# Kernel optimization log

Measured on AMD Instinct MI355X. Metric: run time of the kernel, lower is better.

Reference implementation:

```python
import jax, jax.numpy as jnp
import numpy as np

N_E, E_DIM = 8192, 256
COMMIT = 0.25
DECAY = 0.95
EPS = 1e-05


def setup_inputs() -> dict:
    key = jax.random.key(0)
    k1, k2, k3 = jax.random.split(key, 3)
    x = jax.random.normal(k1, (8, 256, 16, 16, 16), dtype=jnp.float32)
    codebook = jax.random.normal(k2, (N_E, E_DIM), dtype=jnp.float32)
    ema_count = jnp.zeros((N_E,), dtype=jnp.float32)
    ema_weight = jax.random.normal(k3, (N_E, E_DIM), dtype=jnp.float32)
    return {"x": x, "codebook": codebook, "ema_count": ema_count, "ema_weight": ema_weight}


def reference(x, codebook, ema_count, ema_weight):
    b, c, h, w, l = x.shape
    K = codebook.shape[0]
    # 'b c h w l -> (b h w l) c'
    flat_x = jnp.transpose(x, (0, 2, 3, 4, 1)).reshape(-1, c)  # [N, c]
    N = flat_x.shape[0]

    # squared L2 distances via the expanded form (matmul-dominated)
    distances = (jnp.sum(flat_x ** 2, axis=1, keepdims=True)
                 + jnp.sum(codebook ** 2, axis=1)
                 - 2.0 * flat_x @ codebook.T)  # [N, K]
    idx = jnp.argmin(distances, axis=1)  # [N]

    # quantized = one_hot(idx) @ codebook == gather
    quant_flat = codebook[idx]  # [N, c]

    # EMA update (training branch); one-hot column sums == segment sums
    counts = jax.ops.segment_sum(jnp.ones((N,), dtype=x.dtype), idx, num_segments=K)
    new_count = ema_count * DECAY + (1.0 - DECAY) * counts
    new_count = (new_count + EPS) / (b + K * EPS) * b
    dw = jax.ops.segment_sum(flat_x, idx, num_segments=K)  # encodings.T @ flat_x
    new_weight = ema_weight * DECAY + (1.0 - DECAY) * dw
    new_codebook = new_weight / new_count[:, None]

    e_loss = COMMIT * jnp.mean((jax.lax.stop_gradient(quant_flat) - flat_x) ** 2)

    # straight-through estimator
    quant_st = flat_x + jax.lax.stop_gradient(quant_flat - flat_x)
    quantized = jnp.transpose(quant_st.reshape(b, h, w, l, c), (0, 4, 1, 2, 3))

    avg_probs = counts / N
    perplexity = jnp.exp(-jnp.sum(avg_probs * jnp.log(avg_probs + 1e-10)))
    unique = jnp.count_nonzero(counts)

    return (quantized, e_loss, perplexity, unique,
            new_codebook, new_count, new_weight, idx)
```

## Files before the change

### kernel.cpp

```cpp
#include <hip/hip_runtime.h>
#include <hip/hip_bf16.h>
#include <stdint.h>

#define N_ROWS 32768
#define K_CODES 8192
#define C_DIM 256
#define DECAYF 0.95f
#define COMMITF 0.25f
#define EPSF 1e-5f
#define RESC_KEYGAP 2u
#define RESC_CAP 16384

#define OFF_QUANT 0
#define OFF_ELOSS 8388608
#define OFF_PERP  8388609
#define OFF_UNIQ  8388610
#define OFF_NCB   8388611
#define OFF_NCNT  10485763
#define OFF_NW    10493955
#define OFF_IDX   12591107

typedef float f32x4 __attribute__((ext_vector_type(4)));
typedef int i32x4 __attribute__((ext_vector_type(4)));
typedef unsigned long long u64;
typedef unsigned int u32;

#define SWZ(r) ((((r) >> 2) & 7) << 2)

#if defined(__has_builtin)
#if __has_builtin(__builtin_amdgcn_global_load_lds)
#define HAVE_GLDS 1
#endif
#endif
#ifdef HAVE_GLDS
#define GLDS16(g, l) __builtin_amdgcn_global_load_lds( \
    (const __attribute__((address_space(1))) void*)(uintptr_t)(g), \
    (__attribute__((address_space(3))) void*)(uint32_t)(uintptr_t)(l), 16, 0, 0)
#else
#define GLDS16(g, l) do { *(float4*)(l) = *(const float4*)(g); } while (0)
#endif

__device__ __forceinline__ uint32_t fkey(float f) {
    uint32_t b = __float_as_uint(f);
    return b ^ ((uint32_t)((int32_t)b >> 31) | 0x80000000u);
}
__device__ __forceinline__ void enc8(float v, float inv, signed char& h, signed char& l) {
    int q = __float2int_rn(v * inv);
    q = q > 16319 ? 16319 : (q < -16320 ? -16320 : q);
    int hh = (q + 64) >> 7;
    h = (signed char)hh;
    l = (signed char)(q - (hh << 7));
}

__global__ __launch_bounds__(256)
void kmax(const float* __restrict__ x, const float* __restrict__ cb, float* __restrict__ maxbuf) {
    const int bid = blockIdx.x, t = threadIdx.x;
    const float* src = bid < 2048 ? x : cb;
    const size_t base = bid < 2048 ? (size_t)bid * 4096 : (size_t)(bid - 2048) * 4096;
    float m = 0.f;
    #pragma unroll
    for (int i = 0; i < 4; ++i) {
        const float4 v = *(const float4*)(src + base + ((size_t)i * 256 + t) * 4);
        m = fmaxf(m, fmaxf(fmaxf(fabsf(v.x), fabsf(v.y)), fmaxf(fabsf(v.z), fabsf(v.w))));
    }
    #pragma unroll
    for (int off = 32; off; off >>= 1) m = fmaxf(m, __shfl_down(m, off));
    __shared__ float ps[4];
    if ((t & 63) == 0) ps[t >> 6] = m;
    __syncthreads();
    if (t == 0) maxbuf[bid] = fmaxf(fmaxf(ps[0], ps[1]), fmaxf(ps[2], ps[3]));
}

__global__ void kscale(const float* __restrict__ maxbuf, float* __restrict__ scl,
                       float* __restrict__ counts, float* __restrict__ loss_arr,
                       unsigned* __restrict__ rcnt) {
    const int t = threadIdx.x;
    float mx = 0.f, me = 0.f;
    for (int i = t; i < 2048; i += 256) mx = fmaxf(mx, maxbuf[i]);
    for (int i = 2048 + t; i < 2560; i += 256) me = fmaxf(me, maxbuf[i]);
    #pragma unroll
    for (int off = 32; off; off >>= 1) {
        mx = fmaxf(mx, __shfl_down(mx, off));
        me = fmaxf(me, __shfl_down(me, off));
    }
    __shared__ float px[4], pe[4];
    if ((t & 63) == 0) { px[t >> 6] = mx; pe[t >> 6] = me; }
    __syncthreads();
    if (t == 0) {
        const float Sx = fmaxf(fmaxf(px[0], px[1]), fmaxf(px[2], px[3])) * (16384.f / 16320.f) + 1e-20f;
        const float Se = fmaxf(fmaxf(pe[0], pe[1]), fmaxf(pe[2], pe[3])) * (16384.f / 16320.f) + 1e-20f;
        scl[0] = Sx; scl[1] = Se; scl[2] = Sx * Se / 268435456.f;
        *rcnt = 0u;
    }
    for (int i = t; i < K_CODES; i += 256) counts[i] = 0.f;
    loss_arr[t] = 0.f;
}

__global__ __launch_bounds__(256)
void kprep(const float* __restrict__ cb, const float* __restrict__ x,
           signed char* __restrict__ Ah, signed char* __restrict__ Al,
           signed char* __restrict__ Bh, signed char* __restrict__ Bl,
           float* __restrict__ cnorm, const float* __restrict__ scl) {
    const int bid = blockIdx.x;
    const int t = threadIdx.x;
    if (bid < 2048) {
        const float inve = 16384.f / scl[1];
        const size_t i4 = ((size_t)bid * 256 + t) * 4;
        const float4 v = *(const float4*)(cb + i4);
        signed char h0, h1, h2, h3, l0, l1, l2, l3;
        enc8(v.x, inve, h0, l0); enc8(v.y, inve, h1, l1);
        enc8(v.z, inve, h2, l2); enc8(v.w, inve, h3, l3);
        *(char4*)(Bh + i4) = make_char4(h0, h1, h2, h3);
        *(char4*)(Bl + i4) = make_char4(l0, l1, l2, l3);
        float s = v.x * v.x + v.y * v.y + v.z * v.z + v.w * v.w;
        #pragma unroll
        for (int off = 32; off; off >>= 1) s += __shfl_down(s, off);
        if ((t & 63) == 0) cnorm[i4 >> 8] = s;
    } else {
        const float invx = 16384.f / scl[0];
        __shared__ float xt[64][65];
        const int xb_id = bid - 2048;
        const int st = xb_id & 63;
        const int ct = (xb_id >> 6) & 3;
        const int b  = xb_id >> 8;
        const float* xb = x + ((size_t)b * C_DIM + ct * 64) * 4096 + st * 64;
        {
            const int s_l = t & 63, c0 = t >> 6;
            #pragma unroll
            for (int cc = 0; cc < 16; ++cc) {
                int c_l = cc * 4 + c0;
                xt[c_l][s_l] = xb[(size_t)c_l * 4096 + s_l];
            }
        }
        __syncthreads();
        const int c2 = (t & 31) * 2;
        const int s0 = t >> 5;
        #pragma unroll
        for (int ww = 0; ww < 8; ++ww) {
            int s_o = ww * 8 + s0;
            signed char h0, l0, h1, l1;
            enc8(xt[c2][s_o], invx, h0, l0);
            enc8(xt[c2 + 1][s_o], invx, h1, l1);
            size_t off = ((size_t)(b * 4096 + st * 64 + s_o)) * C_DIM + ct * 64 + c2;
            *(char2*)(Ah + off) = make_char2(h0, h1);
            *(char2*)(Al + off) = make_char2(l0, l1);
        }
    }
}

__global__ __launch_bounds__(512, 4)
void kargmin_i8(const signed char* __restrict__ Ah, const signed char* __restrict__ Al,
                const signed char* __restrict__ Bh, const signed char* __restrict__ Bl,
                const float* __restrict__ cnorm, const float* __restrict__ scl,
                uint2* __restrict__ wsmin) {
    __shared__ unsigned char As[3][128 * 64];
    __shared__ unsigned char Bs[3][256 * 64];

    const int t = threadIdx.x;
    const int lane = t & 63;
    const int wid = t >> 6;
    const int xcd = blockIdx.x & 7;
    const int ii = blockIdx.x >> 3;
    const int ntile = xcd * 4 + (ii & 3);
    const int mtile = ii >> 2;
    const int m0 = mtile * 128;
    const int n0 = ntile * 256;
    const int wr = wid >> 2;
    const int wc = wid & 3;
    const int wm = wr * 64;
    const int wn = wc * 64;
    const int lm = lane & 15;
    const int lh = lane >> 4;

    i32x4 acc[4][4];
    #pragma unroll
    for (int i = 0; i < 4; ++i)
        #pragma unroll
        for (int j = 0; j < 4; ++j) acc[i][j] = (i32x4){0, 0, 0, 0};

    const int sAr = t >> 2;
    const int ssl = t & 3;
    const int gsA = ssl ^ (sAr & 3) ^ ((sAr >> 2) & 3);
    const size_t thr = (size_t)sAr * 256 + (size_t)gsA * 16;

    const signed char* pA0 = Ah + (size_t)m0 * 256 + thr;
    const signed char* pA1 = Al + (size_t)m0 * 256 + thr;
    const signed char* pB0 = Bh + (size_t)n0 * 256 + thr;
    const signed char* pB1 = Bl + (size_t)n0 * 256 + thr;

#define STAGE(PA, PB, KOFF, BUF) do { \
        GLDS16((PA) + (KOFF), &As[BUF][t * 16]); \
        GLDS16((PB) + (KOFF), &Bs[BUF][t * 16]); \
        GLDS16((PB) + 32768 + (KOFF), &Bs[BUF][(512 + t) * 16]); \
    } while (0)

#define BARN(N) do { \
        asm volatile("s_waitcnt vmcnt(" #N ")" ::: "memory"); \
        __builtin_amdgcn_sched_barrier(0); \
        __builtin_amdgcn_s_barrier(); \
        __builtin_amdgcn_sched_barrier(0); \
    } while (0)

    const int rboff = (lh ^ (lm & 3) ^ ((lm >> 2) & 3)) * 16;

#define TILEC(CUR, PF, FOLD) do { \
        PF; \
        i32x4 a_[4], b_[4]; \
        _Pragma("unroll") \
        for (int j = 0; j < 4; ++j) \
            b_[j] = *(const i32x4*)&Bs[CUR][(wn + j * 16 + lm) * 64 + rboff]; \
        _Pragma("unroll") \
        for (int i = 0; i < 4; ++i) \
            a_[i] = *(const i32x4*)&As[CUR][(wm + i * 16 + lm) * 64 + rboff]; \
        _Pragma("unroll") \
        for (int i = 0; i < 4; ++i) \
            _Pragma("unroll") \
            for (int j = 0; j < 4; ++j) \
                acc[i][j] = __builtin_amdgcn_mfma_i32_16x16x64_i8(a_[i], b_[j], acc[i][j], 0, 0, 0); \
        FOLD; \
    } while (0)

#define FOLDACC \
        _Pragma("unroll") \
        for (int i = 0; i < 4; ++i) \
            _Pragma("unroll") \
            for (int j = 0; j < 4; ++j) \
                acc[i][j] = acc[i][j] << 7

    STAGE(pA0, pB0, 0, 0);
    STAGE(pA0, pB0, 64, 1);
    BARN(3);
    TILEC(0, STAGE(pA0, pB0, 128, 2), (void)0);  BARN(3);
    TILEC(1, STAGE(pA0, pB0, 192, 0), (void)0);  BARN(3);
    TILEC(2, STAGE(pA0, pB1,   0, 1), (void)0);  BARN(3);
    TILEC(0, STAGE(pA0, pB1,  64, 2), FOLDACC);  BARN(3);
    TILEC(1, STAGE(pA0, pB1, 128, 0), (void)0);  BARN(3);
    TILEC(2, STAGE(pA0, pB1, 192, 1), (void)0);  BARN(3);
    TILEC(0, STAGE(pA1, pB0,   0, 2), (void)0);  BARN(3);
    TILEC(1, STAGE(pA1, pB0,  64, 0), (void)0);  BARN(3);
    TILEC(2, STAGE(pA1, pB0, 128, 1), (void)0);  BARN(3);
    TILEC(0, STAGE(pA1, pB0, 192, 2), (void)0);  BARN(3);
    TILEC(1, (void)0, (void)0);                  BARN(0);
    TILEC(2, (void)0, (void)0);
#undef TILEC
#undef STAGE
#undef BARN
#undef FOLDACC
    __syncthreads();

    const float invu = 1.f / (256.f * scl[2]);
    int cni[4];
    #pragma unroll
    for (int j = 0; j < 4; ++j)
        cni[j] = (int)rintf(cnorm[n0 + wn + j * 16 + lm] * invu) + 0x20000000;

    u32* redbuf = (u32*)&As[0][0];
    #pragma unroll
    for (int i = 0; i < 4; ++i) {
        u32 p1[4], p2[4];
        #pragma unroll
        for (int r = 0; r < 4; ++r) {
            u32 b1 = ~0u, b2 = ~0u;
            #pragma unroll
            for (int j = 0; j < 4; ++j) {
                const u32 v = (u32)(cni[j] - acc[i][j][r]);
                const u32 key = ((v >> 10) << 8) | (u32)(wn + j * 16 + lm);
                if (key < b1) { b2 = b1; b1 = key; }
                else if (key < b2) b2 = key;
            }
            p1[r] = b1; p2[r] = b2;
        }
        #pragma unroll
        for (int off = 1; off < 16; off <<= 1) {
            #pragma unroll
            for (int r = 0; r < 4; ++r) {
                const u32 o1 = __shfl_xor(p1[r], off);
                const u32 o2 = __shfl_xor(p2[r], off);
                const u32 lo = min(p1[r], o1);
                const u32 hi = max(p1[r], o1);
                p1[r] = lo;
                p2[r] = min(hi, min(p2[r], o2));
            }
        }
        if (lm == 0) {
            #pragma unroll
            for (int r = 0; r < 4; ++r) {
                const int rl = wm + i * 16 + lh * 4 + r;
                redbuf[rl * 8 + wc * 2 + 0] = p1[r];
                redbuf[rl * 8 + wc * 2 + 1] = p2[r];
            }
        }
    }
    __syncthreads();
    if (t < 128) {
        u32 m1 = ~0u, m2 = ~0u;
        #pragma unroll
        for (int w = 0; w < 4; ++w) {
            const u32 a1 = redbuf[t * 8 + w * 2 + 0];
            const u32 a2 = redbuf[t * 8 + w * 2 + 1];
            const u32 lo = min(m1, a1);
            const u32 hi = max(m1, a1);
            m1 = lo;
            m2 = min(hi, min(m2, a2));
        }
        wsmin[(size_t)(m0 + t) * 32 + ntile] = make_uint2(m1, m2);
    }
}

__global__ void kcombine(const uint2* __restrict__ wsmin, float* __restrict__ idxf,
                         unsigned* __restrict__ rcnt, unsigned* __restrict__ rrows,
                         uint2* __restrict__ rpair, float* __restrict__ counts) {
    const int row = blockIdx.x * 256 + threadIdx.x;
    const uint2* p = wsmin + (size_t)row * 32;
    u32 m1 = ~0u, m2 = ~0u;
    int nt1 = 0, nt2 = 0;
    for (int nt = 0; nt < 32; ++nt) {
        const uint2 c = p[nt];
        if (c.x < m1) { m2 = m1; nt2 = nt1; m1 = c.x; nt1 = nt; }
        else if (c.x < m2) { m2 = c.x; nt2 = nt; }
        if (c.y < m2) { m2 = c.y; nt2 = nt; }
    }
    const int k = nt1 * 256 + (int)(m1 & 255u);
    idxf[row] = (float)k;
    atomicAdd(&counts[k], 1.0f);
    if ((m2 >> 8) - (m1 >> 8) <= RESC_KEYGAP) {
        unsigned slot = atomicAdd(rcnt, 1u);
        if (slot < RESC_CAP) {
            rrows[slot] = (unsigned)row;
            rpair[slot] = make_uint2((unsigned)k, (unsigned)(nt2 * 256 + (int)(m2 & 255u)));
        }
    }
}

__global__ __launch_bounds__(256)
void krescue2(const float* __restrict__ x, const float* __restrict__ cb,
              const float* __restrict__ cnorm, const unsigned* __restrict__ rcnt,
              const unsigned* __restrict__ rrows, const uint2* __restrict__ rpair,
              float* __restrict__ idxf, float* __restrict__ counts) {
    const int lane = threadIdx.x & 63;
    const int wv = threadIdx.x >> 6;
    unsigned cnt = *rcnt; if (cnt > RESC_CAP) cnt = RESC_CAP;
    for (unsigned i = blockIdx.x * 4 + wv; i < cnt; i += gridDim.x * 4) {
        const int row = (int)rrows[i];
        const uint2 kk = rpair[i];
        const int b = row >> 12, s = row & 4095;
        float d1 = 0.f, d2 = 0.f;
        #pragma unroll
        for (int q = 0; q < 4; ++q) {
            const int c = lane + q * 64;
            const float xv = x[((size_t)(b * 256 + c)) * 4096 + s];
            d1 = fmaf(xv, cb[(size_t)kk.x * 256 + c], d1);
            d2 = fmaf(xv, cb[(size_t)kk.y * 256 + c], d2);
        }
        #pragma unroll
        for (int off = 32; off; off >>= 1) {
            d1 += __shfl_down(d1, off);
            d2 += __shfl_down(d2, off);
        }
        if (lane == 0) {
            const float dist1 = fmaf(-2.f, d1, cnorm[kk.x]);
            const float dist2 = fmaf(-2.f, d2, cnorm[kk.y]);
            const u64 p1 = ((u64)fkey(dist1) << 32) | kk.x;
            const u64 p2 = ((u64)fkey(dist2) << 32) | kk.y;
            const int knew = (int)(unsigned)((p1 < p2 ? p1 : p2) & 0xffffffffu);
            const int kold = (int)kk.x;
            if (knew != kold) {
                atomicAdd(&counts[kold], -1.0f);
                atomicAdd(&counts[knew], 1.0f);
                idxf[row] = (float)knew;
            }
        }
    }
}

__global__ void kscan(const float* __restrict__ counts, unsigned* __restrict__ off,
                      unsigned* __restrict__ cursor) {
    __shared__ unsigned part[256];
    const int t = threadIdx.x;
    unsigned local[32];
    unsigned s = 0;
    #pragma unroll
    for (int i = 0; i < 32; ++i) { local[i] = s; s += (unsigned)counts[t * 32 + i]; }
    part[t] = s;
    __syncthreads();
    if (t == 0) {
        unsigned run = 0;
        for (int i = 0; i < 256; ++i) { unsigned v = part[i]; part[i] = run; run += v; }
    }
    __syncthreads();
    const unsigned base = part[t];
    #pragma unroll
    for (int i = 0; i < 32; ++i) {
        unsigned o = base + local[i];
        off[t * 32 + i] = o;
        cursor[t * 32 + i] = o;
    }
}

__global__ void kscatter(const float* __restrict__ idxf, unsigned* __restrict__ cursor,
                         unsigned* __restrict__ rowlist) {
    const int n = blockIdx.x * 256 + threadIdx.x;
    const int k = (int)idxf[n];
    unsigned pos = atomicAdd(&cursor[k], 1u);
    rowlist[pos] = (unsigned)n;
}

__global__ __launch_bounds__(256)
void kquant2(const float* __restrict__ x, const float* __restrict__ cb,
             const float* __restrict__ idxf, float* __restrict__ qout,
             float* __restrict__ loss_arr) {
    __shared__ int ki[64];
    __shared__ float cbt[64][257];
    const int t = threadIdx.x;
    const int bid = blockIdx.x;
    const int chunk = bid & 63;
    const int b = bid >> 6;
    const int s0 = chunk * 64;
    if (t < 64) ki[t] = (int)idxf[b * 4096 + s0 + t];
    __syncthreads();
    {
        const int lane = t & 63;
        const int rr = t >> 6;
        #pragma unroll
        for (int p = 0; p < 16; ++p) {
            const int r = p * 4 + rr;
            const float4 v = *(const float4*)(cb + (size_t)ki[r] * C_DIM + lane * 4);
            cbt[r][lane * 4 + 0] = v.x;
            cbt[r][lane * 4 + 1] = v.y;
            cbt[r][lane * 4 + 2] = v.z;
            cbt[r][lane * 4 + 3] = v.w;
        }
    }
    __syncthreads();
    const int sg = t & 15;
    const int c0 = t >> 4;
    float lsum = 0.f;
    #pragma unroll
    for (int cc = 0; cc < 16; ++cc) {
        const int c = cc * 16 + c0;
        const size_t go = ((size_t)b * C_DIM + c) * 4096 + s0 + sg * 4;
        const float4 xv = *(const float4*)(x + go);
        float qx = cbt[sg * 4 + 0][c];
        float qy = cbt[sg * 4 + 1][c];
        float qz = cbt[sg * 4 + 2][c];
        float qw = cbt[sg * 4 + 3][c];
        float4 st;
        st.x = xv.x + (qx - xv.x);
        st.y = xv.y + (qy - xv.y);
        st.z = xv.z + (qz - xv.z);
        st.w = xv.w + (qw - xv.w);
        *(float4*)(qout + go) = st;
        float dx = qx - xv.x, dy = qy - xv.y, dz = qz - xv.z, dw_ = qw - xv.w;
        lsum += dx * dx + dy * dy + dz * dz + dw_ * dw_;
    }
    #pragma unroll
    for (int off = 32; off; off >>= 1) lsum += __shfl_down(lsum, off);
    __shared__ float ps[4];
    if ((t & 63) == 0) ps[t >> 6] = lsum;
    __syncthreads();
    if (t == 0) atomicAdd(&loss_arr[bid & 255], ps[0] + ps[1] + ps[2] + ps[3]);
}

__global__ void kfinal3(const float* __restrict__ ema_c, const float* __restrict__ ema_w,
                        const float* __restrict__ counts, const unsigned* __restrict__ off,
                        const unsigned* __restrict__ rowlist,
                        const signed char* __restrict__ Ah, const signed char* __restrict__ Al,
                        const float* __restrict__ scl,
                        float* __restrict__ nw, float* __restrict__ ncb,
                        float* __restrict__ ncnt_out,
                        const float* __restrict__ loss_arr, float* __restrict__ out) {
    const int k = blockIdx.x;
    const int t = threadIdx.x;
    if (k < K_CODES) {
        const int cnt = (int)counts[k];
        const unsigned base = off[k];
        int a = 0;
        for (int i = 0; i < cnt; ++i) {
            const unsigned row = rowlist[base + i];
            a += (int)Ah[(size_t)row * C_DIM + t] * 128 + (int)Al[(size_t)row * C_DIM + t];
        }
        const float dwv = (float)a * (scl[0] * (1.f / 16384.f));
        const float ncnt = (DECAYF * ema_c[k] + (1.f - DECAYF) * counts[k] + EPSF)
                           / (8.f + (float)K_CODES * EPSF) * 8.f;
        const size_t o = (size_t)k * C_DIM + t;
        const float nwv = DECAYF * ema_w[o] + (1.f - DECAYF) * dwv;
        nw[o]  = nwv;
        ncb[o] = nwv / ncnt;
        if (t == 0) ncnt_out[k] = ncnt;
    } else {
        float nz = 0.f, s = 0.f;
        for (int kk = t; kk < K_CODES; kk += 256) {
            float cnt = counts[kk];
            if (cnt != 0.f) nz += 1.f;
            float p = cnt * (1.f / 32768.f);
            s += p * logf(p + 1e-10f);
        }
        float ls = loss_arr[t];
        #pragma unroll
        for (int off_ = 32; off_; off_ >>= 1) {
            s  += __shfl_down(s, off_);
            nz += __shfl_down(nz, off_);
            ls += __shfl_down(ls, off_);
        }
        __shared__ float ss[4], zz[4], ll[4];
        const int wid = t >> 6, lane = t & 63;
        if (lane == 0) { ss[wid] = s; zz[wid] = nz; ll[wid] = ls; }
        __syncthreads();
        if (t == 0) {
            float st = ss[0] + ss[1] + ss[2] + ss[3];
            float zt = zz[0] + zz[1] + zz[2] + zz[3];
            float lt = ll[0] + ll[1] + ll[2] + ll[3];
            out[OFF_ELOSS] = COMMITF * lt / 8388608.f;
            out[OFF_PERP]  = expf(-st);
            out[OFF_UNIQ]  = zt;
        }
    }
}

__global__ void knorm(const float* __restrict__ cb, float* __restrict__ cnorm) {
    const int wid  = threadIdx.x >> 6;
    const int lane = threadIdx.x & 63;
    const int row  = blockIdx.x * 4 + wid;
    const float4 v = *(const float4*)(cb + (size_t)row * C_DIM + lane * 4);
    float s = v.x * v.x + v.y * v.y + v.z * v.z + v.w * v.w;
    #pragma unroll
    for (int off = 32; off; off >>= 1) s += __shfl_down(s, off);
    if (lane == 0) cnorm[row] = s;
}

__launch_bounds__(256, 1)
__global__ void kargmin_fp32(const float* __restrict__ x, const float* __restrict__ cb,
                             const float* __restrict__ cnorm, float* __restrict__ idxf) {
    __shared__ float xs[64][256];
    __shared__ float es[64][256];
    const int t  = threadIdx.x;
    const int n0 = blockIdx.x * 64;
    const int b  = n0 >> 12;
    const int s0 = n0 & 4095;
    {
        const int r  = t & 63;
        const int c0 = t >> 6;
        const float* xb = x + (size_t)b * C_DIM * 4096 + s0 + r;
        const int sw = SWZ(r);
        #pragma unroll 8
        for (int cc = 0; cc < 64; ++cc) {
            int c = cc * 4 + c0;
            xs[r][c ^ sw] = xb[(size_t)c * 4096];
        }
    }
    const int mg  = t >> 4;
    const int ng  = t & 15;
    const int m0  = mg * 4;
    const int nn0 = ng * 4;
    const int swm = SWZ(m0);
    const int swn = SWZ(nn0);
    float minv[4] = {1e30f, 1e30f, 1e30f, 1e30f};
    int   mini[4] = {0, 0, 0, 0};
    for (int k0 = 0; k0 < K_CODES; k0 += 64) {
        __syncthreads();
        {
            const int lane = t & 63;
            const int cw   = t >> 6;
            #pragma unroll
            for (int p = 0; p < 16; ++p) {
                int code = p * 4 + cw;
                float4 v = *(const float4*)(cb + (size_t)(k0 + code) * C_DIM + lane * 4);
                *(float4*)&es[code][(lane * 4) ^ SWZ(code)] = v;
            }
        }
        float cn[4];
        #pragma unroll
        for (int j = 0; j < 4; ++j) cn[j] = cnorm[k0 + nn0 + j];
        __syncthreads();
        float acc[4][4];
        #pragma unroll
        for (int i = 0; i < 4; ++i)
            #pragma unroll
            for (int j = 0; j < 4; ++j) acc[i][j] = 0.f;
        #pragma unroll 4
        for (int c = 0; c < C_DIM; c += 4) {
            float4 xa[4], eb[4];
            #pragma unroll
            for (int i = 0; i < 4; ++i) xa[i] = *(const float4*)&xs[m0 + i][c ^ swm];
            #pragma unroll
            for (int j = 0; j < 4; ++j) eb[j] = *(const float4*)&es[nn0 + j][c ^ swn];
            #pragma unroll
            for (int i = 0; i < 4; ++i)
                #pragma unroll
                for (int j = 0; j < 4; ++j)
                    acc[i][j] += xa[i].x * eb[j].x + xa[i].y * eb[j].y +
                                 xa[i].z * eb[j].z + xa[i].w * eb[j].w;
        }
        #pragma unroll
        for (int j = 0; j < 4; ++j) {
            const int kg = k0 + nn0 + j;
            #pragma unroll
            for (int i = 0; i < 4; ++i) {
                float dist = fmaf(-2.f, acc[i][j], cn[j]);
                if (dist < minv[i]) { minv[i] = dist; mini[i] = kg; }
            }
        }
    }
    #pragma unroll
    for (int off = 1; off < 16; off <<= 1) {
        #pragma unroll
        for (int i = 0; i < 4; ++i) {
            float ov = __shfl_xor(minv[i], off);
            int   oi = __shfl_xor(mini[i], off);
            if (ov < minv[i] || (ov == minv[i] && oi < mini[i])) { minv[i] = ov; mini[i] = oi; }
        }
    }
    if (ng == 0) {
        #pragma unroll
        for (int i = 0; i < 4; ++i) idxf[n0 + m0 + i] = (float)mini[i];
    }
}

__global__ void kquant_legacy(const float* __restrict__ x, const float* __restrict__ cb,
                              const float* __restrict__ idxf, float* __restrict__ qout,
                              float* __restrict__ dw, float* __restrict__ counts,
                              float* __restrict__ loss_arr) {
    const int t   = threadIdx.x;
    const int bid = blockIdx.x;
    const int sc  = bid & 15;
    const int c   = (bid >> 4) & 255;
    const int b   = bid >> 12;
    const int s   = sc * 256 + t;
    const int n   = b * 4096 + s;
    const int k   = (int)idxf[n];
    const size_t xoff = ((size_t)b * C_DIM + c) * 4096 + s;
    const float xv = x[xoff];
    const float q  = cb[(size_t)k * C_DIM + c];
    qout[xoff] = xv + (q - xv);
    atomicAdd(&dw[(size_t)k * C_DIM + c], xv);
    if (c == 0) atomicAdd(&counts[k], 1.0f);
    float d = q - xv;
    float p = d * d;
    #pragma unroll
    for (int off = 32; off; off >>= 1) p += __shfl_down(p, off);
    __shared__ float ps[4];
    if ((t & 63) == 0) ps[t >> 6] = p;
    __syncthreads();
    if (t == 0) atomicAdd(&loss_arr[bid & 255], ps[0] + ps[1] + ps[2] + ps[3]);
}

__global__ void kstats_legacy(const float* __restrict__ counts, const float* __restrict__ loss_arr,
                              float* __restrict__ out) {
    const int t = threadIdx.x;
    float nz = 0.f, s = 0.f;
    for (int k = t; k < K_CODES; k += 256) {
        float cnt = counts[k];
        if (cnt != 0.f) nz += 1.f;
        float p = cnt * (1.f / 32768.f);
        s += p * logf(p + 1e-10f);
    }
    float ls = loss_arr[t];
    #pragma unroll
    for (int off = 32; off; off >>= 1) {
        s  += __shfl_down(s, off);
        nz += __shfl_down(nz, off);
        ls += __shfl_down(ls, off);
    }
    __shared__ float ss[4], zz[4], ll[4];
    const int wid = t >> 6, lane = t & 63;
    if (lane == 0) { ss[wid] = s; zz[wid] = nz; ll[wid] = ls; }
    __syncthreads();
    if (t == 0) {
        out[OFF_ELOSS] = COMMITF * (ll[0] + ll[1] + ll[2] + ll[3]) / 8388608.f;
        out[OFF_PERP]  = expf(-(ss[0] + ss[1] + ss[2] + ss[3]));
        out[OFF_UNIQ]  = zz[0] + zz[1] + zz[2] + zz[3];
    }
}

__global__ void kfinal_legacy(const float* __restrict__ ema_c, const float* __restrict__ ema_w,
                              float* __restrict__ counts, float* __restrict__ dw,
                              float* __restrict__ ncb) {
    const int k = blockIdx.x;
    const int c = threadIdx.x;
    const float cnt  = counts[k];
    const float ncnt = (DECAYF * ema_c[k] + (1.f - DECAYF) * cnt + EPSF)
                       / (8.f + (float)K_CODES * EPSF) * 8.f;
    const size_t o = (size_t)k * C_DIM + c;
    const float nw = DECAYF * ema_w[o] + (1.f - DECAYF) * dw[o];
    __syncthreads();
    dw[o]  = nw;
    ncb[o] = nw / ncnt;
    if (c == 0) counts[k] = ncnt;
}

extern "C" void kernel_launch(void* const* d_in, const int* in_sizes, int n_in,
                              void* d_out, int out_size, void* d_ws, size_t ws_size,
                              hipStream_t stream) {
    const float* x     = (const float*)d_in[0];
    const float* cb    = (const float*)d_in[1];
    const float* ema_c = (const float*)d_in[2];
    const float* ema_w = (const float*)d_in[3];
    float* out = (float*)d_out;

    float* qout = out + OFF_QUANT;
    float* ncb  = out + OFF_NCB;
    float* ncnt = out + OFF_NCNT;
    float* nw   = out + OFF_NW;
    float* idxf = out + OFF_IDX;

    const size_t szA = (size_t)N_ROWS * C_DIM;
    const size_t szB = (size_t)K_CODES * C_DIM;
    const size_t fcount = 8192 + 256 + 8192 + 4 + 2560;
    const size_t need = 2 * szA + 2 * szB + fcount * 4
                      + RESC_CAP * 8 + RESC_CAP * 4 + 4 + 8192 * 4 * 2 + 32768 * 4 + 64;
    const bool use_i8 = ws_size >= need;

    if (use_i8) {
        signed char* Ah = (signed char*)d_ws;
        signed char* Al = Ah + szA;
        signed char* Bh = Al + szA;
        signed char* Bl = Bh + szB;
        float* fbase      = (float*)(Bl + szB);
        float* cnorm      = fbase;
        float* loss_arr   = fbase + 8192;
        float* counts_raw = fbase + 8448;
        float* scl        = fbase + 16640;
        float* maxbuf     = fbase + 16644;
        uint2* rpair      = (uint2*)(fbase + fcount);
        unsigned* rrows   = (unsigned*)(rpair + RESC_CAP);
        unsigned* rcnt    = rrows + RESC_CAP;
        unsigned* off     = rcnt + 1;
        unsigned* cursor  = off + K_CODES;
        unsigned* rowlist = cursor + K_CODES;
        uint2* wsmin = (uint2*)(out + OFF_QUANT);

        kmax<<<2560, 256, 0, stream>>>(x, cb, maxbuf);
        kscale<<<1, 256, 0, stream>>>(maxbuf, scl, counts_raw, loss_arr, rcnt);
        kprep<<<4096, 256, 0, stream>>>(cb, x, Ah, Al, Bh, Bl, cnorm, scl);
        kargmin_i8<<<8192, 512, 0, stream>>>(Ah, Al, Bh, Bl, cnorm, scl, wsmin);
        kcombine<<<N_ROWS / 256, 256, 0, stream>>>(wsmin, idxf, rcnt, rrows, rpair, counts_raw);
        krescue2<<<256, 256, 0, stream>>>(x, cb, cnorm, rcnt, rrows, rpair, idxf, counts_raw);
        kscan<<<1, 256, 0, stream>>>(counts_raw, off, cursor);
        kscatter<<<N_ROWS / 256, 256, 0, stream>>>(idxf, cursor, rowlist);
        kquant2<<<512, 256, 0, stream>>>(x, cb, idxf, qout, loss_arr);
        kfinal3<<<K_CODES + 1, C_DIM, 0, stream>>>(ema_c, ema_w, counts_raw, off, rowlist,
                                                   Ah, Al, scl, nw, ncb, ncnt, loss_arr, out);
    } else {
        float* cnorm = (float*)d_ws;
        float* loss_arr = cnorm + K_CODES;
        hipMemsetAsync(ncnt, 0, K_CODES * sizeof(float), stream);
        hipMemsetAsync(nw, 0, (size_t)K_CODES * C_DIM * sizeof(float), stream);
        hipMemsetAsync(loss_arr, 0, 256 * sizeof(float), stream);
        knorm<<<K_CODES / 4, 256, 0, stream>>>(cb, cnorm);
        kargmin_fp32<<<N_ROWS / 64, 256, 0, stream>>>(x, cb, cnorm, idxf);
        kquant_legacy<<<32768, 256, 0, stream>>>(x, cb, idxf, qout, nw, ncnt, loss_arr);
        kstats_legacy<<<1, 256, 0, stream>>>(ncnt, loss_arr, out);
        kfinal_legacy<<<K_CODES, C_DIM, 0, stream>>>(ema_c, ema_w, ncnt, nw, ncb);
    }
}
```

Before: 463.8 us.

## Fuse rescue pass into combine kernel and raise MFMA wave priority

Merges the near-tie rescue recomputation into the combine kernel, so each block collects its ambiguous rows in LDS and rechecks them locally. This drops one kernel launch and the global atomic queue with its capacity cap. It also wraps the int8 MFMA loop in s_setprio to favour matrix issue. In exchange, rescue work is now spread unevenly across blocks and holds up any block that has many ambiguous rows.

```diff
diff --git a/kernel.cpp b/kernel.cpp
--- a/kernel.cpp
+++ b/kernel.cpp
@@ -212,11 +212,13 @@
         _Pragma("unroll") \
         for (int i = 0; i < 4; ++i) \
             a_[i] = *(const i32x4*)&As[CUR][(wm + i * 16 + lm) * 64 + rboff]; \
+        __builtin_amdgcn_s_setprio(1); \
         _Pragma("unroll") \
         for (int i = 0; i < 4; ++i) \
             _Pragma("unroll") \
             for (int j = 0; j < 4; ++j) \
                 acc[i][j] = __builtin_amdgcn_mfma_i32_16x16x64_i8(a_[i], b_[j], acc[i][j], 0, 0, 0); \
+        __builtin_amdgcn_s_setprio(0); \
         FOLD; \
     } while (0)
 
@@ -307,10 +309,18 @@
     }
 }
 
-__global__ void kcombine(const uint2* __restrict__ wsmin, float* __restrict__ idxf,
-                         unsigned* __restrict__ rcnt, unsigned* __restrict__ rrows,
-                         uint2* __restrict__ rpair, float* __restrict__ counts) {
-    const int row = blockIdx.x * 256 + threadIdx.x;
+__global__ __launch_bounds__(256)
+void kcombine(const uint2* __restrict__ wsmin, float* __restrict__ idxf,
+              const float* __restrict__ x, const float* __restrict__ cb,
+              const float* __restrict__ cnorm, float* __restrict__ counts) {
+    __shared__ unsigned frow[256];
+    __shared__ uint2 fpair[256];
+    __shared__ unsigned fn;
+    const int t = threadIdx.x;
+    if (t == 0) fn = 0u;
+    __syncthreads();
+
+    const int row = blockIdx.x * 256 + t;
     const uint2* p = wsmin + (size_t)row * 32;
     u32 m1 = ~0u, m2 = ~0u;
     int nt1 = 0, nt2 = 0;
@@ -324,26 +334,19 @@
     idxf[row] = (float)k;
     atomicAdd(&counts[k], 1.0f);
     if ((m2 >> 8) - (m1 >> 8) <= RESC_KEYGAP) {
-        unsigned slot = atomicAdd(rcnt, 1u);
-        if (slot < RESC_CAP) {
-            rrows[slot] = (unsigned)row;
-            rpair[slot] = make_uint2((unsigned)k, (unsigned)(nt2 * 256 + (int)(m2 & 255u)));
-        }
-    }
-}
-
-__global__ __launch_bounds__(256)
-void krescue2(const float* __restrict__ x, const float* __restrict__ cb,
-              const float* __restrict__ cnorm, const unsigned* __restrict__ rcnt,
-              const unsigned* __restrict__ rrows, const uint2* __restrict__ rpair,
-              float* __restrict__ idxf, float* __restrict__ counts) {
-    const int lane = threadIdx.x & 63;
-    const int wv = threadIdx.x >> 6;
-    unsigned cnt = *rcnt; if (cnt > RESC_CAP) cnt = RESC_CAP;
-    for (unsigned i = blockIdx.x * 4 + wv; i < cnt; i += gridDim.x * 4) {
-        const int row = (int)rrows[i];
-        const uint2 kk = rpair[i];
-        const int b = row >> 12, s = row & 4095;
+        const unsigned slot = atomicAdd(&fn, 1u);
+        frow[slot] = (unsigned)row;
+        fpair[slot] = make_uint2((unsigned)k, (unsigned)(nt2 * 256 + (int)(m2 & 255u)));
+    }
+    __syncthreads();
+
+    const unsigned nf = fn;
+    const int lane = t & 63;
+    const int wv = t >> 6;
+    for (unsigned i = wv; i < nf; i += 4) {
+        const int row2 = (int)frow[i];
+        const uint2 kk = fpair[i];
+        const int b = row2 >> 12, s = row2 & 4095;
         float d1 = 0.f, d2 = 0.f;
         #pragma unroll
         for (int q = 0; q < 4; ++q) {
@@ -367,7 +370,7 @@
             if (knew != kold) {
                 atomicAdd(&counts[kold], -1.0f);
                 atomicAdd(&counts[knew], 1.0f);
-                idxf[row] = (float)knew;
+                idxf[row2] = (float)knew;
             }
         }
     }
@@ -733,8 +736,7 @@
         kscale<<<1, 256, 0, stream>>>(maxbuf, scl, counts_raw, loss_arr, rcnt);
         kprep<<<4096, 256, 0, stream>>>(cb, x, Ah, Al, Bh, Bl, cnorm, scl);
         kargmin_i8<<<8192, 512, 0, stream>>>(Ah, Al, Bh, Bl, cnorm, scl, wsmin);
-        kcombine<<<N_ROWS / 256, 256, 0, stream>>>(wsmin, idxf, rcnt, rrows, rpair, counts_raw);
-        krescue2<<<256, 256, 0, stream>>>(x, cb, cnorm, rcnt, rrows, rpair, idxf, counts_raw);
+        kcombine<<<N_ROWS / 256, 256, 0, stream>>>(wsmin, idxf, x, cb, cnorm, counts_raw);
         kscan<<<1, 256, 0, stream>>>(counts_raw, off, cursor);
         kscatter<<<N_ROWS / 256, 256, 0, stream>>>(idxf, cursor, rowlist);
         kquant2<<<512, 256, 0, stream>>>(x, cb, idxf, qout, loss_arr);
```

New measurement: 452.3 us. 2.5% less time.
